# Kernel tuning notes

Hardware: AMD Instinct MI355X
Metric: run time of the kernel (lower is better)

## Reference

```python
import jax, jax.numpy as jnp
import numpy as np

N = 100000      # nodes
E = 625000      # edges
F_IN = 128      # num_features
C = 32          # num_classes


def setup_inputs() -> dict:
    key = jax.random.key(0)
    k1, k2, k3, k4, k5 = jax.random.split(key, 5)
    x = jax.random.normal(k1, (N, F_IN), dtype=jnp.float32)
    edge_index = jax.random.randint(k2, (2, E), 0, N, dtype=jnp.int64)
    s = 1.0 / np.sqrt(F_IN)
    # PyG SAGEConv: lin_l (applied to aggregated neighbors, with bias), lin_r (applied to self, no bias)
    W_l = jax.random.uniform(k3, (C, F_IN), dtype=jnp.float32, minval=-s, maxval=s)
    b_l = jax.random.uniform(k4, (C,), dtype=jnp.float32, minval=-s, maxval=s)
    W_r = jax.random.uniform(k5, (C, F_IN), dtype=jnp.float32, minval=-s, maxval=s)
    return {"x": x, "edge_index": edge_index, "W_l": W_l, "b_l": b_l, "W_r": W_r}


def reference(x, edge_index, W_l, b_l, W_r):
    src, dst = edge_index[0], edge_index[1]
    # mean aggregation of source-node features at destination nodes
    msg_sum = jax.ops.segment_sum(x[src], dst, num_segments=N)            # [N, F]
    deg = jax.ops.segment_sum(jnp.ones((E,), x.dtype), dst, num_segments=N)
    agg = msg_sum / jnp.maximum(deg, 1.0)[:, None]
    # SAGEConv: lin_l(agg) + lin_r(x)
    h = agg @ W_l.T + b_l + x @ W_r.T                                     # [N, C]
    h = jax.nn.relu(h)
    # dropout is identity in eval mode
    return jax.nn.log_softmax(h, axis=1)
```

## Files before the change

### kernel.cpp

```cpp
#include <hip/hip_runtime.h>
#include <hip/hip_fp16.h>
#include <math.h>

#define F_IN 128
#define NCLS 32
#define CAP  32
#define NPART 8
#define PADW 136

typedef __attribute__((ext_vector_type(8))) short short8v;
typedef __attribute__((ext_vector_type(4))) float f32x4;

__device__ __forceinline__ unsigned int pk2(float lo, float hi) {
    unsigned int a = __float_as_uint(lo), b = __float_as_uint(hi);
    a = (a + 0x7fffu + ((a >> 16) & 1u)) >> 16;
    b = (b + 0x7fffu + ((b >> 16) & 1u)) >> 16;
    return a | (b << 16);
}
__device__ __forceinline__ uint4 pack8(float4 a, float4 b) {
    return make_uint4(pk2(a.x, a.y), pk2(a.z, a.w), pk2(b.x, b.y), pk2(b.z, b.w));
}

__global__ __launch_bounds__(256) void proj_kernel(const float* __restrict__ x,
                                                   const float* __restrict__ Wl,
                                                   const float* __restrict__ Wr,
                                                   __half* __restrict__ zl,
                                                   __half* __restrict__ zr,
                                                   int* __restrict__ cnt, int N) {
    __shared__ __align__(16) unsigned short xs[64 * PADW];
    __shared__ __align__(16) unsigned short ws[64 * PADW];
    int t = threadIdx.x;
    int node0 = blockIdx.x * 64;

    if (t < 64) {
        int n = node0 + t;
        if (n < N) cnt[n] = 0;
    }

    #pragma unroll
    for (int p = 0; p < 4; ++p) {
        int idx = t + p * 256;
        int row = idx >> 4;
        int q   = idx & 15;

        const float* srcW = (row < NCLS) ? (Wl + row * F_IN) : (Wr + (row - NCLS) * F_IN);
        float4 wa = *(const float4*)(srcW + q * 8);
        float4 wb = *(const float4*)(srcW + q * 8 + 4);
        *(uint4*)(ws + row * PADW + q * 8) = pack8(wa, wb);

        int node = node0 + row;
        int safe = (node < N) ? node : (N - 1);
        const float* srcX = x + (size_t)safe * F_IN;
        float4 xa = *(const float4*)(srcX + q * 8);
        float4 xb = *(const float4*)(srcX + q * 8 + 4);
        *(uint4*)(xs + row * PADW + q * 8) = pack8(xa, xb);
    }
    __syncthreads();

    int wave = t >> 6;
    int lane = t & 63;
    int l15  = lane & 15;
    int koff = (lane >> 4) * 8;

    f32x4 acc[4] = {{0.f,0.f,0.f,0.f},{0.f,0.f,0.f,0.f},{0.f,0.f,0.f,0.f},{0.f,0.f,0.f,0.f}};
    const unsigned short* xrow = xs + (wave * 16 + l15) * PADW + koff;
    const unsigned short* wrow = ws + l15 * PADW + koff;

    #pragma unroll
    for (int ks = 0; ks < 4; ++ks) {
        short8v a = *reinterpret_cast<const short8v*>(xrow + ks * 32);
        #pragma unroll
        for (int ct = 0; ct < 4; ++ct) {
            short8v b = *reinterpret_cast<const short8v*>(wrow + ct * 16 * PADW + ks * 32);
            acc[ct] = __builtin_amdgcn_mfma_f32_16x16x32_bf16(a, b, acc[ct], 0, 0, 0);
        }
    }

    int r0 = (lane >> 4) * 4;
    #pragma unroll
    for (int ct = 0; ct < 4; ++ct) {
        __half* zp = (ct < 2) ? zl : zr;
        int cc = (ct & 1) * 16 + l15;
        #pragma unroll
        for (int r = 0; r < 4; ++r) {
            int node = node0 + wave * 16 + r0 + r;
            if (node < N) zp[(size_t)node * NCLS + cc] = __float2half(acc[ct][r]);
        }
    }
}

__global__ __launch_bounds__(256) void fill_kernel(const void* __restrict__ ei,
                                                   int* __restrict__ cnt,
                                                   int* __restrict__ col,
                                                   int E, int N, int span) {
    const unsigned int* u32 = (const unsigned int*)ei;
    unsigned int aa = 0;
    #pragma unroll
    for (int j = 0; j < 16; ++j) aa |= u32[2 * j + 1];
    int is64 = (aa == 0u);

    int part = blockIdx.x & (NPART - 1);
    int e0 = ((blockIdx.x >> 3) * 256 + threadIdx.x) * 4;
    if (e0 >= E) return;
    int lo = part * span;
    int hi = lo + span; if (hi > N) hi = N;
    int ecnt = (E - e0 >= 4) ? 4 : (E - e0);

    int d[4];
    if (is64) {
        const long long* dp = (const long long*)ei + E + e0;
        if (ecnt == 4) {
            longlong2 d01 = *(const longlong2*)dp, d23 = *(const longlong2*)(dp + 2);
            d[0]=(int)d01.x; d[1]=(int)d01.y; d[2]=(int)d23.x; d[3]=(int)d23.y;
        } else {
            for (int j = 0; j < ecnt; ++j) d[j] = (int)dp[j];
        }
    } else {
        const int* dp = (const int*)ei + E + e0;
        if (ecnt == 4) {
            int4 dv = *(const int4*)dp;
            d[0]=dv.x; d[1]=dv.y; d[2]=dv.z; d[3]=dv.w;
        } else {
            for (int j = 0; j < ecnt; ++j) d[j] = dp[j];
        }
    }

    for (int j = 0; j < ecnt; ++j) {
        if (d[j] >= lo && d[j] < hi) {
            int sv = is64 ? (int)((const long long*)ei)[e0 + j]
                          : ((const int*)ei)[e0 + j];
            if ((unsigned)sv >= (unsigned)N) sv = 0;
            int pos = atomicAdd(&cnt[d[j]], 1);
            if (pos < CAP) col[(size_t)d[j] * CAP + pos] = sv;
        }
    }
}

__global__ __launch_bounds__(256) void finish_kernel(const __half* __restrict__ zl,
                                                     const __half* __restrict__ zr,
                                                     const int* __restrict__ col,
                                                     const int* __restrict__ cnt,
                                                     const float* __restrict__ bl,
                                                     float* __restrict__ out, int N) {
    int gid = blockIdx.x * 256 + threadIdx.x;
    int node = gid >> 5;
    int c = gid & 31;
    if (node >= N) return;

    int deg = cnt[node];
    int m = (deg < CAP) ? deg : CAP;
    const int* cb = col + (size_t)node * CAP;
    float selfz = __half2float(zr[(size_t)node * NCLS + c]);
    float bias  = bl[c];

    float a[8] = {};
    for (int base = 0; base < m; base += 8) {
        int4 n0 = *(const int4*)(cb + base);
        int4 n1 = *(const int4*)(cb + base + 4);
        int idx[8] = {n0.x, n0.y, n0.z, n0.w, n1.x, n1.y, n1.z, n1.w};
        #pragma unroll
        for (int k = 0; k < 8; ++k) {
            bool ok = (base + k < m);
            int s = ok ? idx[k] : 0;
            float v = __half2float(zl[(size_t)s * NCLS + c]);
            a[k] += ok ? v : 0.f;
        }
    }
    float acc = ((a[0] + a[1]) + (a[2] + a[3])) + ((a[4] + a[5]) + (a[6] + a[7]));

    float inv = 1.0f / fmaxf((float)deg, 1.0f);
    float h = acc * inv + bias + selfz;
    h = fmaxf(h, 0.f);

    float mx = h;
    #pragma unroll
    for (int o = 16; o >= 1; o >>= 1) mx = fmaxf(mx, __shfl_xor(mx, o));
    float p = h - mx;
    float ex = __expf(p);
    float s = ex;
    #pragma unroll
    for (int o = 16; o >= 1; o >>= 1) s += __shfl_xor(s, o);

    out[(size_t)node * NCLS + c] = p - __logf(s);
}

__global__ void detect_i64_kernel(const unsigned int* __restrict__ ei, int* __restrict__ flag) {
    if (blockIdx.x == 0 && threadIdx.x == 0) {
        unsigned int acc = 0;
        #pragma unroll
        for (int i = 0; i < 64; ++i) acc |= ei[2 * i + 1];
        *flag = (acc == 0u) ? 1 : 0;
    }
}

__global__ __launch_bounds__(256) void scatter_kernel(const float* __restrict__ x,
                                                      const void* __restrict__ ei,
                                                      const int* __restrict__ flag,
                                                      float* __restrict__ msg,
                                                      float* __restrict__ deg, int E, int N) {
    long long gid = (long long)blockIdx.x * blockDim.x + threadIdx.x;
    int e = (int)(gid >> 5);
    if (e >= E) return;
    int c = (int)(gid & 31);
    int is64 = *flag;
    int src = is64 ? (int)((const long long*)ei)[e] : ((const int*)ei)[e];
    int dst = is64 ? (int)((const long long*)ei)[(size_t)E + e] : ((const int*)ei)[(size_t)E + e];
    if ((unsigned)src >= (unsigned)N || (unsigned)dst >= (unsigned)N) return;
    float4 v = *(const float4*)(x + (size_t)src * F_IN + (c << 2));
    float* m = msg + (size_t)dst * F_IN + (c << 2);
    atomicAdd(m + 0, v.x);
    atomicAdd(m + 1, v.y);
    atomicAdd(m + 2, v.z);
    atomicAdd(m + 3, v.w);
    if (c == 0) atomicAdd(deg + dst, 1.0f);
}

__global__ __launch_bounds__(256) void apply_kernel(const float* __restrict__ x,
                                                    const float* __restrict__ msg,
                                                    const float* __restrict__ degf,
                                                    const float* __restrict__ Wl,
                                                    const float* __restrict__ bl,
                                                    const float* __restrict__ Wr,
                                                    float* __restrict__ out, int N) {
    int n = blockIdx.x * 256 + threadIdx.x;
    if (n >= N) return;
    float inv = 1.0f / fmaxf(degf[n], 1.0f);
    float acc[NCLS];
    #pragma unroll
    for (int c = 0; c < NCLS; ++c) acc[c] = bl[c];
    const float* xr = x + (size_t)n * F_IN;
    const float* mr = msg + (size_t)n * F_IN;
    for (int kb = 0; kb < F_IN; kb += 4) {
        float4 xv = *(const float4*)(xr + kb);
        float4 mv = *(const float4*)(mr + kb);
        float b0 = mv.x * inv, b1 = mv.y * inv, b2 = mv.z * inv, b3 = mv.w * inv;
        #pragma unroll
        for (int c = 0; c < NCLS; ++c) {
            float4 wl = *(const float4*)(Wl + c * F_IN + kb);
            float4 wr = *(const float4*)(Wr + c * F_IN + kb);
            acc[c] += b0 * wl.x + b1 * wl.y + b2 * wl.z + b3 * wl.w
                    + xv.x * wr.x + xv.y * wr.y + xv.z * wr.z + xv.w * wr.w;
        }
    }
    float mx = 0.0f;
    #pragma unroll
    for (int c = 0; c < NCLS; ++c) { acc[c] = fmaxf(acc[c], 0.0f); mx = fmaxf(mx, acc[c]); }
    float s = 0.0f;
    #pragma unroll
    for (int c = 0; c < NCLS; ++c) s += __expf(acc[c] - mx);
    float lg = __logf(s);
    float* o = out + (size_t)n * NCLS;
    #pragma unroll
    for (int q = 0; q < NCLS; q += 4) {
        float4 w = make_float4(acc[q] - mx - lg, acc[q + 1] - mx - lg,
                               acc[q + 2] - mx - lg, acc[q + 3] - mx - lg);
        *(float4*)(o + q) = w;
    }
}

extern "C" void kernel_launch(void* const* d_in, const int* in_sizes, int n_in,
                              void* d_out, int out_size, void* d_ws, size_t ws_size,
                              hipStream_t stream) {
    const float* x  = (const float*)d_in[0];
    const void*  ei = d_in[1];
    const float* Wl = (const float*)d_in[2];
    const float* bl = (const float*)d_in[3];
    const float* Wr = (const float*)d_in[4];

    int N = in_sizes[0] / F_IN;
    int E = in_sizes[1] / 2;
    int span = (N + NPART - 1) / NPART;

    size_t need = (size_t)N * NCLS * 2 * 2 + (size_t)N * 4 + (size_t)N * CAP * 4;

    if (ws_size >= need) {
        __half* zl  = (__half*)d_ws;
        __half* zr  = zl + (size_t)N * NCLS;
        int*    cnt = (int*)(zr + (size_t)N * NCLS);
        int*    col = cnt + N;
        float*  outp = (float*)d_out;

        int T  = (N + 63) / 64;
        int FU = ((E + 1023) / 1024) * NPART;

        proj_kernel<<<T, 256, 0, stream>>>(x, Wl, Wr, zl, zr, cnt, N);
        fill_kernel<<<FU, 256, 0, stream>>>(ei, cnt, col, E, N, span);
        long long tot = (long long)N * 32;
        finish_kernel<<<(int)((tot + 255) / 256), 256, 0, stream>>>(zl, zr, col, cnt, bl,
                                                                    outp, N);
    } else {
        float* msg  = (float*)d_ws;
        float* deg  = msg + (size_t)N * F_IN;
        int*   flag = (int*)(deg + N);

        hipMemsetAsync(d_ws, 0, ((size_t)N * F_IN + N) * 4, stream);
        detect_i64_kernel<<<1, 64, 0, stream>>>((const unsigned int*)ei, flag);

        long long tot = (long long)E * 32;
        scatter_kernel<<<(int)((tot + 255) / 256), 256, 0, stream>>>(x, ei, flag, msg, deg, E, N);
        apply_kernel<<<(N + 255) / 256, 256, 0, stream>>>(x, msg, deg, Wl, bl, Wr,
                                                          (float*)d_out, N);
    }
}
```

Baseline: 68.45 us.

## Merge projection and edge-fill into one launch, pre-pack weights once

Splits the old projection kernel into a tiny init kernel and a combined kernel. The init kernel zeroes the degree counters and converts W_l/W_r to bf16 once into workspace. The combined kernel runs edge-fill blocks and projection blocks in a single grid, so the atomic-heavy CSR fill can overlap the MFMA projection instead of running after it. Each projection block now reads pre-packed weights from global memory rather than converting them per block, which frees half its shared memory. The cost is one extra small launch and weight reads from global or L2 instead of LDS.

```diff
diff --git a/kernel.cpp b/kernel.cpp
--- a/kernel.cpp
+++ b/kernel.cpp
@@ -21,86 +21,36 @@
     return make_uint4(pk2(a.x, a.y), pk2(a.z, a.w), pk2(b.x, b.y), pk2(b.z, b.w));
 }
 
-__global__ __launch_bounds__(256) void proj_kernel(const float* __restrict__ x,
-                                                   const float* __restrict__ Wl,
+__global__ __launch_bounds__(256) void init_kernel(const float* __restrict__ Wl,
                                                    const float* __restrict__ Wr,
-                                                   __half* __restrict__ zl,
-                                                   __half* __restrict__ zr,
+                                                   unsigned short* __restrict__ wb,
                                                    int* __restrict__ cnt, int N) {
-    __shared__ __align__(16) unsigned short xs[64 * PADW];
-    __shared__ __align__(16) unsigned short ws[64 * PADW];
     int t = threadIdx.x;
-    int node0 = blockIdx.x * 64;
-
-    if (t < 64) {
-        int n = node0 + t;
-        if (n < N) cnt[n] = 0;
-    }
-
-    #pragma unroll
-    for (int p = 0; p < 4; ++p) {
-        int idx = t + p * 256;
+    int b = blockIdx.x;
+    int i = b * 256 + t;
+    if (i < N) cnt[i] = 0;
+    if (b < 4) {
+        int idx = b * 256 + t;
         int row = idx >> 4;
         int q   = idx & 15;
-
         const float* srcW = (row < NCLS) ? (Wl + row * F_IN) : (Wr + (row - NCLS) * F_IN);
-        float4 wa = *(const float4*)(srcW + q * 8);
-        float4 wb = *(const float4*)(srcW + q * 8 + 4);
-        *(uint4*)(ws + row * PADW + q * 8) = pack8(wa, wb);
-
-        int node = node0 + row;
-        int safe = (node < N) ? node : (N - 1);
-        const float* srcX = x + (size_t)safe * F_IN;
-        float4 xa = *(const float4*)(srcX + q * 8);
-        float4 xb = *(const float4*)(srcX + q * 8 + 4);
-        *(uint4*)(xs + row * PADW + q * 8) = pack8(xa, xb);
-    }
-    __syncthreads();
-
-    int wave = t >> 6;
-    int lane = t & 63;
-    int l15  = lane & 15;
-    int koff = (lane >> 4) * 8;
-
-    f32x4 acc[4] = {{0.f,0.f,0.f,0.f},{0.f,0.f,0.f,0.f},{0.f,0.f,0.f,0.f},{0.f,0.f,0.f,0.f}};
-    const unsigned short* xrow = xs + (wave * 16 + l15) * PADW + koff;
-    const unsigned short* wrow = ws + l15 * PADW + koff;
-
-    #pragma unroll
-    for (int ks = 0; ks < 4; ++ks) {
-        short8v a = *reinterpret_cast<const short8v*>(xrow + ks * 32);
-        #pragma unroll
-        for (int ct = 0; ct < 4; ++ct) {
-            short8v b = *reinterpret_cast<const short8v*>(wrow + ct * 16 * PADW + ks * 32);
-            acc[ct] = __builtin_amdgcn_mfma_f32_16x16x32_bf16(a, b, acc[ct], 0, 0, 0);
-        }
-    }
-
-    int r0 = (lane >> 4) * 4;
-    #pragma unroll
-    for (int ct = 0; ct < 4; ++ct) {
-        __half* zp = (ct < 2) ? zl : zr;
-        int cc = (ct & 1) * 16 + l15;
-        #pragma unroll
-        for (int r = 0; r < 4; ++r) {
-            int node = node0 + wave * 16 + r0 + r;
-            if (node < N) zp[(size_t)node * NCLS + cc] = __float2half(acc[ct][r]);
-        }
-    }
-}
-
-__global__ __launch_bounds__(256) void fill_kernel(const void* __restrict__ ei,
-                                                   int* __restrict__ cnt,
-                                                   int* __restrict__ col,
-                                                   int E, int N, int span) {
+        float4 a = *(const float4*)(srcW + q * 8);
+        float4 bb = *(const float4*)(srcW + q * 8 + 4);
+        *(uint4*)(wb + row * F_IN + q * 8) = pack8(a, bb);
+    }
+}
+
+__device__ __forceinline__ void dev_fill_unit(const void* __restrict__ ei,
+                                              int* __restrict__ cnt, int* __restrict__ col,
+                                              int E, int N, int span, int u, int t) {
     const unsigned int* u32 = (const unsigned int*)ei;
     unsigned int aa = 0;
     #pragma unroll
     for (int j = 0; j < 16; ++j) aa |= u32[2 * j + 1];
     int is64 = (aa == 0u);
 
-    int part = blockIdx.x & (NPART - 1);
-    int e0 = ((blockIdx.x >> 3) * 256 + threadIdx.x) * 4;
+    int part = u & (NPART - 1);
+    int e0 = ((u >> 3) * 256 + t) * 4;
     if (e0 >= E) return;
     int lo = part * span;
     int hi = lo + span; if (hi > N) hi = N;
@@ -132,6 +82,71 @@
             if ((unsigned)sv >= (unsigned)N) sv = 0;
             int pos = atomicAdd(&cnt[d[j]], 1);
             if (pos < CAP) col[(size_t)d[j] * CAP + pos] = sv;
+        }
+    }
+}
+
+__global__ __launch_bounds__(256) void projfill_kernel(const float* __restrict__ x,
+                                                       const void* __restrict__ ei,
+                                                       const unsigned short* __restrict__ wb,
+                                                       __half* __restrict__ zl,
+                                                       __half* __restrict__ zr,
+                                                       int* __restrict__ cnt,
+                                                       int* __restrict__ col,
+                                                       int N, int E, int span, int FU) {
+    __shared__ __align__(16) unsigned short xs[64 * PADW];
+    int t = threadIdx.x;
+    int b = blockIdx.x;
+
+    if (b < FU) {
+        dev_fill_unit(ei, cnt, col, E, N, span, b, t);
+        return;
+    }
+
+    int node0 = (b - FU) * 64;
+
+    #pragma unroll
+    for (int p = 0; p < 4; ++p) {
+        int idx = t + p * 256;
+        int row = idx >> 4;
+        int q   = idx & 15;
+        int node = node0 + row;
+        int safe = (node < N) ? node : (N - 1);
+        const float* srcX = x + (size_t)safe * F_IN;
+        float4 xa = *(const float4*)(srcX + q * 8);
+        float4 xb = *(const float4*)(srcX + q * 8 + 4);
+        *(uint4*)(xs + row * PADW + q * 8) = pack8(xa, xb);
+    }
+    __syncthreads();
+
+    int wave = t >> 6;
+    int lane = t & 63;
+    int l15  = lane & 15;
+    int koff = (lane >> 4) * 8;
+
+    f32x4 acc[4] = {{0.f,0.f,0.f,0.f},{0.f,0.f,0.f,0.f},{0.f,0.f,0.f,0.f},{0.f,0.f,0.f,0.f}};
+    const unsigned short* xrow = xs + (wave * 16 + l15) * PADW + koff;
+    const unsigned short* wrow = wb + l15 * F_IN + koff;
+
+    #pragma unroll
+    for (int ks = 0; ks < 4; ++ks) {
+        short8v a = *reinterpret_cast<const short8v*>(xrow + ks * 32);
+        #pragma unroll
+        for (int ct = 0; ct < 4; ++ct) {
+            short8v bfr = *reinterpret_cast<const short8v*>(wrow + ct * 16 * F_IN + ks * 32);
+            acc[ct] = __builtin_amdgcn_mfma_f32_16x16x32_bf16(a, bfr, acc[ct], 0, 0, 0);
+        }
+    }
+
+    int r0 = (lane >> 4) * 4;
+    #pragma unroll
+    for (int ct = 0; ct < 4; ++ct) {
+        __half* zp = (ct < 2) ? zl : zr;
+        int cc = (ct & 1) * 16 + l15;
+        #pragma unroll
+        for (int r = 0; r < 4; ++r) {
+            int node = node0 + wave * 16 + r0 + r;
+            if (node < N) zp[(size_t)node * NCLS + cc] = __float2half(acc[ct][r]);
         }
     }
 }
@@ -271,20 +286,24 @@
     int E = in_sizes[1] / 2;
     int span = (N + NPART - 1) / NPART;
 
-    size_t need = (size_t)N * NCLS * 2 * 2 + (size_t)N * 4 + (size_t)N * CAP * 4;
+    size_t need = (size_t)N * NCLS * 2 * 2 + (size_t)N * 4 + (size_t)N * CAP * 4 + 64 * F_IN * 2;
 
     if (ws_size >= need) {
         __half* zl  = (__half*)d_ws;
         __half* zr  = zl + (size_t)N * NCLS;
         int*    cnt = (int*)(zr + (size_t)N * NCLS);
         int*    col = cnt + N;
+        unsigned short* wb = (unsigned short*)(col + (size_t)N * CAP);
         float*  outp = (float*)d_out;
 
         int T  = (N + 63) / 64;
         int FU = ((E + 1023) / 1024) * NPART;
-
-        proj_kernel<<<T, 256, 0, stream>>>(x, Wl, Wr, zl, zr, cnt, N);
-        fill_kernel<<<FU, 256, 0, stream>>>(ei, cnt, col, E, N, span);
+        int NB = (N + 255) / 256;
+        if (NB < 4) NB = 4;
+
+        init_kernel<<<NB, 256, 0, stream>>>(Wl, Wr, wb, cnt, N);
+        projfill_kernel<<<FU + T, 256, 0, stream>>>(x, ei, wb, zl, zr, cnt, col,
+                                                    N, E, span, FU);
         long long tot = (long long)N * 32;
         finish_kernel<<<(int)((tot + 255) / 256), 256, 0, stream>>>(zl, zr, col, cnt, bl,
                                                                     outp, N);
```

Measured after the change: 78.27 us. +14.3%, slower.

## Shard per-node neighbor lists across eight slots to reduce atomic contention

Applied to the files above, without the earlier changes.

Instead of filtering edges by destination range in eight passes over the edge list, each edge is read once and appended to one of eight per-node shards (chosen by block index), each with its own counter and capacity of ten. The finish kernel walks all eight shards, summing the counts for the degree and gathering neighbors. This removes the repeated edge reads and spreads atomics across shards. In exchange the counter and column arrays grow eightfold, the finish kernel issues many more count and index loads per node, and neighbors beyond ten in a shard are dropped.

```diff
diff --git a/kernel.cpp b/kernel.cpp
--- a/kernel.cpp
+++ b/kernel.cpp
@@ -4,8 +4,8 @@
 
 #define F_IN 128
 #define NCLS 32
-#define CAP  32
-#define NPART 8
+#define NSH  8
+#define SCAP 10
 #define PADW 136
 
 typedef __attribute__((ext_vector_type(8))) short short8v;
@@ -32,9 +32,12 @@
     int t = threadIdx.x;
     int node0 = blockIdx.x * 64;
 
-    if (t < 64) {
-        int n = node0 + t;
-        if (n < N) cnt[n] = 0;
+    #pragma unroll
+    for (int k = 0; k < 2; ++k) {
+        int i = t + k * 256;
+        int s = i >> 6;
+        int n = node0 + (i & 63);
+        if (n < N) cnt[(size_t)s * N + n] = 0;
     }
 
     #pragma unroll
@@ -91,54 +94,36 @@
 
 __global__ __launch_bounds__(256) void fill_kernel(const void* __restrict__ ei,
                                                    int* __restrict__ cnt,
-                                                   int* __restrict__ col,
-                                                   int E, int N, int span) {
+                                                   int* __restrict__ colx,
+                                                   int E, int N) {
     const unsigned int* u32 = (const unsigned int*)ei;
     unsigned int aa = 0;
     #pragma unroll
     for (int j = 0; j < 16; ++j) aa |= u32[2 * j + 1];
     int is64 = (aa == 0u);
 
-    int part = blockIdx.x & (NPART - 1);
-    int e0 = ((blockIdx.x >> 3) * 256 + threadIdx.x) * 4;
-    if (e0 >= E) return;
-    int lo = part * span;
-    int hi = lo + span; if (hi > N) hi = N;
-    int ecnt = (E - e0 >= 4) ? 4 : (E - e0);
-
-    int d[4];
+    int s = blockIdx.x & (NSH - 1);
+    int e = blockIdx.x * 256 + threadIdx.x;
+    if (e >= E) return;
+
+    int dd, sv;
     if (is64) {
-        const long long* dp = (const long long*)ei + E + e0;
-        if (ecnt == 4) {
-            longlong2 d01 = *(const longlong2*)dp, d23 = *(const longlong2*)(dp + 2);
-            d[0]=(int)d01.x; d[1]=(int)d01.y; d[2]=(int)d23.x; d[3]=(int)d23.y;
-        } else {
-            for (int j = 0; j < ecnt; ++j) d[j] = (int)dp[j];
-        }
+        dd = (int)((const long long*)ei)[(size_t)E + e];
+        sv = (int)((const long long*)ei)[e];
     } else {
-        const int* dp = (const int*)ei + E + e0;
-        if (ecnt == 4) {
-            int4 dv = *(const int4*)dp;
-            d[0]=dv.x; d[1]=dv.y; d[2]=dv.z; d[3]=dv.w;
-        } else {
-            for (int j = 0; j < ecnt; ++j) d[j] = dp[j];
-        }
-    }
-
-    for (int j = 0; j < ecnt; ++j) {
-        if (d[j] >= lo && d[j] < hi) {
-            int sv = is64 ? (int)((const long long*)ei)[e0 + j]
-                          : ((const int*)ei)[e0 + j];
-            if ((unsigned)sv >= (unsigned)N) sv = 0;
-            int pos = atomicAdd(&cnt[d[j]], 1);
-            if (pos < CAP) col[(size_t)d[j] * CAP + pos] = sv;
-        }
-    }
+        dd = ((const int*)ei)[(size_t)E + e];
+        sv = ((const int*)ei)[e];
+    }
+    if ((unsigned)dd >= (unsigned)N) return;
+    if ((unsigned)sv >= (unsigned)N) sv = 0;
+
+    int pos = atomicAdd(&cnt[(size_t)s * N + dd], 1);
+    if (pos < SCAP) colx[((size_t)s * N + dd) * SCAP + pos] = sv;
 }
 
 __global__ __launch_bounds__(256) void finish_kernel(const __half* __restrict__ zl,
                                                      const __half* __restrict__ zr,
-                                                     const int* __restrict__ col,
+                                                     const int* __restrict__ colx,
                                                      const int* __restrict__ cnt,
                                                      const float* __restrict__ bl,
                                                      float* __restrict__ out, int N) {
@@ -147,26 +132,34 @@
     int c = gid & 31;
     if (node >= N) return;
 
-    int deg = cnt[node];
-    int m = (deg < CAP) ? deg : CAP;
-    const int* cb = col + (size_t)node * CAP;
     float selfz = __half2float(zr[(size_t)node * NCLS + c]);
     float bias  = bl[c];
 
-    float a[8] = {};
-    for (int base = 0; base < m; base += 8) {
-        int4 n0 = *(const int4*)(cb + base);
-        int4 n1 = *(const int4*)(cb + base + 4);
-        int idx[8] = {n0.x, n0.y, n0.z, n0.w, n1.x, n1.y, n1.z, n1.w};
-        #pragma unroll
-        for (int k = 0; k < 8; ++k) {
-            bool ok = (base + k < m);
-            int s = ok ? idx[k] : 0;
-            float v = __half2float(zl[(size_t)s * NCLS + c]);
-            a[k] += ok ? v : 0.f;
-        }
-    }
-    float acc = ((a[0] + a[1]) + (a[2] + a[3])) + ((a[4] + a[5]) + (a[6] + a[7]));
+    int deg = 0;
+    float a[SCAP] = {};
+    #pragma unroll
+    for (int sh = 0; sh < NSH; ++sh) {
+        int cs = cnt[(size_t)sh * N + node];
+        deg += cs;
+        if (cs > SCAP) cs = SCAP;
+        const int* cb = colx + ((size_t)sh * N + node) * SCAP;
+        int2 p0 = *(const int2*)(cb + 0);
+        int2 p1 = *(const int2*)(cb + 2);
+        int2 p2 = *(const int2*)(cb + 4);
+        int2 p3 = *(const int2*)(cb + 6);
+        int2 p4 = *(const int2*)(cb + 8);
+        int id[SCAP] = {p0.x, p0.y, p1.x, p1.y, p2.x, p2.y, p3.x, p3.y, p4.x, p4.y};
+        #pragma unroll
+        for (int j = 0; j < SCAP; ++j) {
+            bool ok = (j < cs);
+            int sv = ok ? id[j] : 0;
+            float v = __half2float(zl[(size_t)sv * NCLS + c]);
+            a[j] += ok ? v : 0.f;
+        }
+    }
+    float acc = 0.f;
+    #pragma unroll
+    for (int j = 0; j < SCAP; ++j) acc += a[j];
 
     float inv = 1.0f / fmaxf((float)deg, 1.0f);
     float h = acc * inv + bias + selfz;
@@ -269,24 +262,24 @@
 
     int N = in_sizes[0] / F_IN;
     int E = in_sizes[1] / 2;
-    int span = (N + NPART - 1) / NPART;
-
-    size_t need = (size_t)N * NCLS * 2 * 2 + (size_t)N * 4 + (size_t)N * CAP * 4;
+
+    size_t need = (size_t)N * NCLS * 2 * 2 + (size_t)N * NSH * 4
+                + (size_t)N * NSH * SCAP * 4;
 
     if (ws_size >= need) {
-        __half* zl  = (__half*)d_ws;
-        __half* zr  = zl + (size_t)N * NCLS;
-        int*    cnt = (int*)(zr + (size_t)N * NCLS);
-        int*    col = cnt + N;
+        __half* zl   = (__half*)d_ws;
+        __half* zr   = zl + (size_t)N * NCLS;
+        int*    cnt  = (int*)(zr + (size_t)N * NCLS);
+        int*    colx = cnt + (size_t)N * NSH;
         float*  outp = (float*)d_out;
 
         int T  = (N + 63) / 64;
-        int FU = ((E + 1023) / 1024) * NPART;
+        int EB = (E + 255) / 256;
 
         proj_kernel<<<T, 256, 0, stream>>>(x, Wl, Wr, zl, zr, cnt, N);
-        fill_kernel<<<FU, 256, 0, stream>>>(ei, cnt, col, E, N, span);
+        fill_kernel<<<EB, 256, 0, stream>>>(ei, cnt, colx, E, N);
         long long tot = (long long)N * 32;
-        finish_kernel<<<(int)((tot + 255) / 256), 256, 0, stream>>>(zl, zr, col, cnt, bl,
+        finish_kernel<<<(int)((tot + 255) / 256), 256, 0, stream>>>(zl, zr, colx, cnt, bl,
                                                                     outp, N);
     } else {
         float* msg  = (float*)d_ws;
```

New measurement: 124.5 us. 81.9% more time.

## Merge projection and CSR fill into one launch with half-K LDS staging

Applied to the files above, without the earlier changes.

Moves count zeroing into its own small kernel, then merges the projection GEMM and the edge-bucketing fill into one grid. Block IDs below T do the projection and the rest do the fill, so memory-bound atomics overlap with the MFMA work. The projection now stages K in two 64-wide halves, which halves LDS use and should raise occupancy, at the cost of an extra barrier and reload pass. It adds one kernel launch, and the fill's atomics now compete with projection traffic.

```diff
diff --git a/kernel.cpp b/kernel.cpp
--- a/kernel.cpp
+++ b/kernel.cpp
@@ -6,7 +6,7 @@
 #define NCLS 32
 #define CAP  32
 #define NPART 8
-#define PADW 136
+#define PADH 72
 
 typedef __attribute__((ext_vector_type(8))) short short8v;
 typedef __attribute__((ext_vector_type(4))) float f32x4;
@@ -21,58 +21,115 @@
     return make_uint4(pk2(a.x, a.y), pk2(a.z, a.w), pk2(b.x, b.y), pk2(b.z, b.w));
 }
 
-__global__ __launch_bounds__(256) void proj_kernel(const float* __restrict__ x,
-                                                   const float* __restrict__ Wl,
-                                                   const float* __restrict__ Wr,
-                                                   __half* __restrict__ zl,
-                                                   __half* __restrict__ zr,
-                                                   int* __restrict__ cnt, int N) {
-    __shared__ __align__(16) unsigned short xs[64 * PADW];
-    __shared__ __align__(16) unsigned short ws[64 * PADW];
+__global__ __launch_bounds__(256) void zero_kernel(int* __restrict__ cnt, int N) {
+    int i = blockIdx.x * 256 + threadIdx.x;
+    if (i < N) cnt[i] = 0;
+}
+
+__global__ __launch_bounds__(256) void projfill_kernel(const float* __restrict__ x,
+                                                       const void* __restrict__ ei,
+                                                       const float* __restrict__ Wl,
+                                                       const float* __restrict__ Wr,
+                                                       __half* __restrict__ zl,
+                                                       __half* __restrict__ zr,
+                                                       int* __restrict__ cnt,
+                                                       int* __restrict__ col,
+                                                       int N, int E, int span, int T) {
+    __shared__ __align__(16) unsigned short xs[64 * PADH];
+    __shared__ __align__(16) unsigned short ws[64 * PADH];
     int t = threadIdx.x;
-    int node0 = blockIdx.x * 64;
-
-    if (t < 64) {
-        int n = node0 + t;
-        if (n < N) cnt[n] = 0;
-    }
-
-    #pragma unroll
-    for (int p = 0; p < 4; ++p) {
-        int idx = t + p * 256;
-        int row = idx >> 4;
-        int q   = idx & 15;
-
-        const float* srcW = (row < NCLS) ? (Wl + row * F_IN) : (Wr + (row - NCLS) * F_IN);
-        float4 wa = *(const float4*)(srcW + q * 8);
-        float4 wb = *(const float4*)(srcW + q * 8 + 4);
-        *(uint4*)(ws + row * PADW + q * 8) = pack8(wa, wb);
-
-        int node = node0 + row;
-        int safe = (node < N) ? node : (N - 1);
-        const float* srcX = x + (size_t)safe * F_IN;
-        float4 xa = *(const float4*)(srcX + q * 8);
-        float4 xb = *(const float4*)(srcX + q * 8 + 4);
-        *(uint4*)(xs + row * PADW + q * 8) = pack8(xa, xb);
-    }
-    __syncthreads();
-
+    int b = blockIdx.x;
+
+    if (b >= T) {
+        int u = b - T;
+        const unsigned int* u32 = (const unsigned int*)ei;
+        unsigned int aa = 0;
+        #pragma unroll
+        for (int j = 0; j < 16; ++j) aa |= u32[2 * j + 1];
+        int is64 = (aa == 0u);
+
+        int part = u & (NPART - 1);
+        int e0 = ((u >> 3) * 256 + t) * 4;
+        if (e0 >= E) return;
+        int lo = part * span;
+        int hi = lo + span; if (hi > N) hi = N;
+        int ecnt = (E - e0 >= 4) ? 4 : (E - e0);
+
+        int d[4];
+        if (is64) {
+            const long long* dp = (const long long*)ei + E + e0;
+            if (ecnt == 4) {
+                longlong2 d01 = *(const longlong2*)dp, d23 = *(const longlong2*)(dp + 2);
+                d[0]=(int)d01.x; d[1]=(int)d01.y; d[2]=(int)d23.x; d[3]=(int)d23.y;
+            } else {
+                for (int j = 0; j < ecnt; ++j) d[j] = (int)dp[j];
+            }
+        } else {
+            const int* dp = (const int*)ei + E + e0;
+            if (ecnt == 4) {
+                int4 dv = *(const int4*)dp;
+                d[0]=dv.x; d[1]=dv.y; d[2]=dv.z; d[3]=dv.w;
+            } else {
+                for (int j = 0; j < ecnt; ++j) d[j] = dp[j];
+            }
+        }
+
+        for (int j = 0; j < ecnt; ++j) {
+            if (d[j] >= lo && d[j] < hi) {
+                int sv = is64 ? (int)((const long long*)ei)[e0 + j]
+                              : ((const int*)ei)[e0 + j];
+                if ((unsigned)sv >= (unsigned)N) sv = 0;
+                int pos = atomicAdd(&cnt[d[j]], 1);
+                if (pos < CAP) col[(size_t)d[j] * CAP + pos] = sv;
+            }
+        }
+        return;
+    }
+
+    int node0 = b * 64;
     int wave = t >> 6;
     int lane = t & 63;
     int l15  = lane & 15;
     int koff = (lane >> 4) * 8;
 
     f32x4 acc[4] = {{0.f,0.f,0.f,0.f},{0.f,0.f,0.f,0.f},{0.f,0.f,0.f,0.f},{0.f,0.f,0.f,0.f}};
-    const unsigned short* xrow = xs + (wave * 16 + l15) * PADW + koff;
-    const unsigned short* wrow = ws + l15 * PADW + koff;
-
-    #pragma unroll
-    for (int ks = 0; ks < 4; ++ks) {
-        short8v a = *reinterpret_cast<const short8v*>(xrow + ks * 32);
-        #pragma unroll
-        for (int ct = 0; ct < 4; ++ct) {
-            short8v b = *reinterpret_cast<const short8v*>(wrow + ct * 16 * PADW + ks * 32);
-            acc[ct] = __builtin_amdgcn_mfma_f32_16x16x32_bf16(a, b, acc[ct], 0, 0, 0);
+
+    #pragma unroll
+    for (int kh = 0; kh < 2; ++kh) {
+        int k0 = kh * 64;
+        if (kh) __syncthreads();
+
+        #pragma unroll
+        for (int p = 0; p < 2; ++p) {
+            int idx = t + p * 256;
+            int row = idx >> 3;
+            int q   = idx & 7;
+
+            const float* srcW = (row < NCLS) ? (Wl + row * F_IN) : (Wr + (row - NCLS) * F_IN);
+            float4 wa = *(const float4*)(srcW + k0 + q * 8);
+            float4 wb = *(const float4*)(srcW + k0 + q * 8 + 4);
+            *(uint4*)(ws + row * PADH + q * 8) = pack8(wa, wb);
+
+            int node = node0 + row;
+            int safe = (node < N) ? node : (N - 1);
+            const float* srcX = x + (size_t)safe * F_IN;
+            float4 xa = *(const float4*)(srcX + k0 + q * 8);
+            float4 xb = *(const float4*)(srcX + k0 + q * 8 + 4);
+            *(uint4*)(xs + row * PADH + q * 8) = pack8(xa, xb);
+        }
+        __syncthreads();
+
+        const unsigned short* xrow = xs + (wave * 16 + l15) * PADH + koff;
+        const unsigned short* wrow = ws + l15 * PADH + koff;
+
+        #pragma unroll
+        for (int ks = 0; ks < 2; ++ks) {
+            short8v a = *reinterpret_cast<const short8v*>(xrow + ks * 32);
+            #pragma unroll
+            for (int ct = 0; ct < 4; ++ct) {
+                short8v bf = *reinterpret_cast<const short8v*>(wrow + ct * 16 * PADH + ks * 32);
+                acc[ct] = __builtin_amdgcn_mfma_f32_16x16x32_bf16(a, bf, acc[ct], 0, 0, 0);
+            }
         }
     }
 
@@ -85,53 +142,6 @@
         for (int r = 0; r < 4; ++r) {
             int node = node0 + wave * 16 + r0 + r;
             if (node < N) zp[(size_t)node * NCLS + cc] = __float2half(acc[ct][r]);
-        }
-    }
-}
-
-__global__ __launch_bounds__(256) void fill_kernel(const void* __restrict__ ei,
-                                                   int* __restrict__ cnt,
-                                                   int* __restrict__ col,
-                                                   int E, int N, int span) {
-    const unsigned int* u32 = (const unsigned int*)ei;
-    unsigned int aa = 0;
-    #pragma unroll
-    for (int j = 0; j < 16; ++j) aa |= u32[2 * j + 1];
-    int is64 = (aa == 0u);
-
-    int part = blockIdx.x & (NPART - 1);
-    int e0 = ((blockIdx.x >> 3) * 256 + threadIdx.x) * 4;
-    if (e0 >= E) return;
-    int lo = part * span;
-    int hi = lo + span; if (hi > N) hi = N;
-    int ecnt = (E - e0 >= 4) ? 4 : (E - e0);
-
-    int d[4];
-    if (is64) {
-        const long long* dp = (const long long*)ei + E + e0;
-        if (ecnt == 4) {
-            longlong2 d01 = *(const longlong2*)dp, d23 = *(const longlong2*)(dp + 2);
-            d[0]=(int)d01.x; d[1]=(int)d01.y; d[2]=(int)d23.x; d[3]=(int)d23.y;
-        } else {
-            for (int j = 0; j < ecnt; ++j) d[j] = (int)dp[j];
-        }
-    } else {
-        const int* dp = (const int*)ei + E + e0;
-        if (ecnt == 4) {
-            int4 dv = *(const int4*)dp;
-            d[0]=dv.x; d[1]=dv.y; d[2]=dv.z; d[3]=dv.w;
-        } else {
-            for (int j = 0; j < ecnt; ++j) d[j] = dp[j];
-        }
-    }
-
-    for (int j = 0; j < ecnt; ++j) {
-        if (d[j] >= lo && d[j] < hi) {
-            int sv = is64 ? (int)((const long long*)ei)[e0 + j]
-                          : ((const int*)ei)[e0 + j];
-            if ((unsigned)sv >= (unsigned)N) sv = 0;
-            int pos = atomicAdd(&cnt[d[j]], 1);
-            if (pos < CAP) col[(size_t)d[j] * CAP + pos] = sv;
         }
     }
 }
@@ -283,8 +293,9 @@
         int T  = (N + 63) / 64;
         int FU = ((E + 1023) / 1024) * NPART;
 
-        proj_kernel<<<T, 256, 0, stream>>>(x, Wl, Wr, zl, zr, cnt, N);
-        fill_kernel<<<FU, 256, 0, stream>>>(ei, cnt, col, E, N, span);
+        zero_kernel<<<(N + 255) / 256, 256, 0, stream>>>(cnt, N);
+        projfill_kernel<<<T + FU, 256, 0, stream>>>(x, ei, Wl, Wr, zl, zr, cnt, col,
+                                                    N, E, span, T);
         long long tot = (long long)N * 32;
         finish_kernel<<<(int)((tot + 255) / 256), 256, 0, stream>>>(zl, zr, col, cnt, bl,
                                                                     outp, N);
```

Result: faster. 66.93 us, median of 2 (-2.2%).
